# Kernel optimization log

Hardware: AMD Instinct MI355X
Metric: run time of the kernel (lower is better)

Reference implementation:

```python
import jax, jax.numpy as jnp
import numpy as np

GRID_SHAPE = (128, 128, 128, 8)
N_POINTS = 2_000_000


def setup_inputs() -> dict:
    key = jax.random.key(0)
    k1, k2 = jax.random.split(key)
    coords = jax.random.uniform(k1, (N_POINTS, 3), dtype=jnp.float32)
    grid = jax.random.normal(k2, GRID_SHAPE, dtype=jnp.float32)
    bbox_min = jnp.zeros((3,), dtype=jnp.float32)
    bbox_max = jnp.ones((3,), dtype=jnp.float32)
    return {"coords": coords, "grid": grid, "bbox_min": bbox_min, "bbox_max": bbox_max}


def reference(coords, grid, bbox_min, bbox_max):
    # coords: [N, 3]; grid: [X, Y, Z, C]
    eps = 1e-06
    coords = coords[:, :3]
    scale = jnp.maximum(bbox_max - bbox_min, eps)
    normalized = jnp.clip((coords - bbox_min) / scale, 0.0, 1.0)
    grid_size = jnp.asarray(grid.shape[:3], dtype=jnp.int64)  # [3]
    pos = normalized * (grid_size.astype(coords.dtype) - 1.0)  # [N, 3]
    idx0 = jnp.floor(pos).astype(jnp.int64)                    # [N, 3]
    idx1 = jnp.minimum(idx0 + 1, grid_size - 1)                # [N, 3]
    weight = jnp.clip(pos - idx0.astype(coords.dtype), 0.0, 1.0)  # [N, 3]

    x0, y0, z0 = idx0[:, 0], idx0[:, 1], idx0[:, 2]
    x1, y1, z1 = idx1[:, 0], idx1[:, 1], idx1[:, 2]
    wx, wy, wz = weight[:, 0:1], weight[:, 1:2], weight[:, 2:3]  # each [N, 1]

    c000 = grid[x0, y0, z0]
    c100 = grid[x1, y0, z0]
    c010 = grid[x0, y1, z0]
    c110 = grid[x1, y1, z0]
    c001 = grid[x0, y0, z1]
    c101 = grid[x1, y0, z1]
    c011 = grid[x0, y1, z1]
    c111 = grid[x1, y1, z1]

    c00 = c000 * (1.0 - wx) + c100 * wx
    c01 = c001 * (1.0 - wx) + c101 * wx
    c10 = c010 * (1.0 - wx) + c110 * wx
    c11 = c011 * (1.0 - wx) + c111 * wx
    c0 = c00 * (1.0 - wy) + c10 * wy
    c1 = c01 * (1.0 - wy) + c11 * wy
    return c0 * (1.0 - wz) + c1 * wz  # [N, C]
```

## Files before the change

### kernel.cpp

```cpp
#include <hip/hip_runtime.h>


#define GS    128
#define NBX   32
#define NB2   4096
#define CAP1  65536
#define CAP2  704
#define K_PTS 1024
#define HCELLS (5 * 5 * 33)

__device__ __forceinline__ void cell_of(
    float cx, float cy, float cz,
    float b0x, float b0y, float b0z,
    float sx, float sy, float sz,
    int& x0, int& y0, int& z0)
{
    float nx = fminf(fmaxf((cx - b0x) / sx, 0.0f), 1.0f);
    float ny = fminf(fmaxf((cy - b0y) / sy, 0.0f), 1.0f);
    float nz = fminf(fmaxf((cz - b0z) / sz, 0.0f), 1.0f);
    x0 = (int)(nx * (float)(GS - 1));
    y0 = (int)(ny * (float)(GS - 1));
    z0 = (int)(nz * (float)(GS - 1));
}

__global__ __launch_bounds__(256) void k_init(
    unsigned* __restrict__ cursor32, unsigned* __restrict__ cursor4096)
{
    int i = blockIdx.x * 256 + threadIdx.x;
    if (i < NBX) cursor32[i] = (unsigned)i * CAP1;
    if (i < NB2) cursor4096[i] = (unsigned)i * CAP2;
}

__global__ __launch_bounds__(256) void k_scatter1(
    const float* __restrict__ coords,
    const float* __restrict__ bbox_min,
    const float* __restrict__ bbox_max,
    unsigned* __restrict__ cursor32,
    float4* __restrict__ recs1, int n)
{
    __shared__ float4 srec[K_PTS];
    __shared__ unsigned char sbkt[K_PTS];
    __shared__ unsigned cnt[NBX], lbase[NBX], gbase[NBX];

    int t = threadIdx.x;
    if (t < NBX) cnt[t] = 0;
    __syncthreads();

    float b0x = bbox_min[0];
    float sx  = fmaxf(bbox_max[0] - b0x, 1e-6f);
    long long base = (long long)blockIdx.x * K_PTS;
    int m = (int)min((long long)K_PTS, (long long)n - base);

    float cx[4], cy[4], cz[4];
    int bb[4]; unsigned rr[4];
    int j0 = 4 * t;
    if (j0 + 3 < m) {
        const float4* c4 = (const float4*)coords + (size_t)blockIdx.x * 768 + 3 * t;
        float4 f0 = c4[0], f1 = c4[1], f2 = c4[2];
        cx[0] = f0.x; cy[0] = f0.y; cz[0] = f0.z;
        cx[1] = f0.w; cy[1] = f1.x; cz[1] = f1.y;
        cx[2] = f1.z; cy[2] = f1.w; cz[2] = f2.x;
        cx[3] = f2.y; cy[3] = f2.z; cz[3] = f2.w;
    } else {
#pragma unroll
        for (int p = 0; p < 4; ++p) {
            int j = j0 + p;
            if (j < m) {
                long long i = base + j;
                cx[p] = coords[3 * i]; cy[p] = coords[3 * i + 1]; cz[p] = coords[3 * i + 2];
            }
        }
    }
#pragma unroll
    for (int p = 0; p < 4; ++p) {
        int j = j0 + p;
        if (j < m) {
            float nx = fminf(fmaxf((cx[p] - b0x) / sx, 0.0f), 1.0f);
            bb[p] = ((int)(nx * (float)(GS - 1))) >> 2;
            rr[p] = atomicAdd(&cnt[bb[p]], 1u);
        }
    }
    __syncthreads();

    if (t == 0) {
        unsigned acc = 0;
        for (int j = 0; j < NBX; ++j) { lbase[j] = acc; acc += cnt[j]; }
    }
    if (t < NBX && cnt[t]) gbase[t] = atomicAdd(&cursor32[t], cnt[t]);
    __syncthreads();

#pragma unroll
    for (int p = 0; p < 4; ++p) {
        int j = j0 + p;
        if (j < m) {
            unsigned slot = lbase[bb[p]] + rr[p];
            float4 r; r.x = cx[p]; r.y = cy[p]; r.z = cz[p];
            r.w = __uint_as_float((unsigned)(base + j));
            srec[slot] = r;
            sbkt[slot] = (unsigned char)bb[p];
        }
    }
    __syncthreads();

#pragma unroll
    for (int k = 0; k < 4; ++k) {
        int j = k * 256 + t;
        if (j < m) {
            int b = sbkt[j];
            unsigned d = gbase[b] + (unsigned)j - lbase[b];
            if (d < (unsigned)(b + 1) * CAP1) recs1[d] = srec[j];
        }
    }
}

__global__ __launch_bounds__(256) void k_scatter2(
    const float4* __restrict__ recs1,
    const float* __restrict__ bbox_min,
    const float* __restrict__ bbox_max,
    const unsigned* __restrict__ cursor32_final,
    unsigned* __restrict__ cursor4096,
    float4* __restrict__ recs2)
{
    __shared__ float4 srec[K_PTS];
    __shared__ unsigned char sbkt[K_PTS];
    __shared__ unsigned cnt[128], lbase[128], gbase[128];

    int s = blockIdx.x >> 6;
    int c = blockIdx.x & 63;
    unsigned fill = cursor32_final[s] - (unsigned)s * CAP1;
    if (fill > CAP1) fill = CAP1;
    unsigned off = (unsigned)c * 1024;
    if (off >= fill) return;
    int m = (int)min(1024u, fill - off);

    int t = threadIdx.x;
    if (t < 128) cnt[t] = 0;
    __syncthreads();

    float b0x = bbox_min[0], b0y = bbox_min[1], b0z = bbox_min[2];
    float sx = fmaxf(bbox_max[0] - b0x, 1e-6f);
    float sy = fmaxf(bbox_max[1] - b0y, 1e-6f);
    float sz = fmaxf(bbox_max[2] - b0z, 1e-6f);
    long long base = (long long)s * CAP1 + off;

    float4 rc[4]; int bb[4]; unsigned rr[4];
#pragma unroll
    for (int k = 0; k < 4; ++k) {
        int j = k * 256 + t;
        if (j < m) {
            rc[k] = recs1[base + j];
            int x0, y0, z0;
            cell_of(rc[k].x, rc[k].y, rc[k].z, b0x, b0y, b0z, sx, sy, sz, x0, y0, z0);
            bb[k] = ((y0 >> 2) << 2) | (z0 >> 5);
            rr[k] = atomicAdd(&cnt[bb[k]], 1u);
        }
    }
    __syncthreads();

    if (t == 0) {
        unsigned acc = 0;
        for (int j = 0; j < 128; ++j) { lbase[j] = acc; acc += cnt[j]; }
    }
    if (t < 128 && cnt[t]) gbase[t] = atomicAdd(&cursor4096[s * 128 + t], cnt[t]);
    __syncthreads();

#pragma unroll
    for (int k = 0; k < 4; ++k) {
        int j = k * 256 + t;
        if (j < m) {
            unsigned slot = lbase[bb[k]] + rr[k];
            srec[slot] = rc[k];
            sbkt[slot] = (unsigned char)bb[k];
        }
    }
    __syncthreads();

#pragma unroll
    for (int k = 0; k < 4; ++k) {
        int j = k * 256 + t;
        if (j < m) {
            int lb = sbkt[j];
            unsigned g = (unsigned)s * 128 + lb;
            unsigned d = gbase[lb] + (unsigned)j - lbase[lb];
            if (d < (g + 1) * CAP2) recs2[d] = srec[j];
        }
    }
}

__global__ __launch_bounds__(512) void k_interp_staged(
    const float4* __restrict__ recs2,
    const unsigned* __restrict__ cursor4096_final,
    const float* __restrict__ grid,
    const float* __restrict__ bbox_min,
    const float* __restrict__ bbox_max,
    float4* __restrict__ out4)
{
    __shared__ float4 tile[HCELLS * 2];
    __shared__ float4 srec[CAP2];

    int ob = blockIdx.x;
    int b  = (ob & 7) * 512 + (ob >> 3);

    unsigned s0 = (unsigned)b * CAP2;
    unsigned e  = cursor4096_final[b];
    unsigned cap_end = s0 + CAP2;
    if (e > cap_end) e = cap_end;
    if (e <= s0) return;
    int cnt = (int)(e - s0);

    int xs = b >> 7, ys = (b >> 2) & 31, zq = b & 3;
    int t = threadIdx.x;

    for (int k = t; k < cnt; k += 512) srec[k] = recs2[s0 + k];

    const float4* g4 = (const float4*)grid;
    for (int k = t; k < HCELLS * 2; k += 512) {
        int c  = k >> 1, half = k & 1;
        int lx = c / 165;
        int r2 = c - lx * 165;
        int ly = r2 / 33;
        int lz = r2 - ly * 33;
        int gx = min(xs * 4 + lx, GS - 1);
        int gy = min(ys * 4 + ly, GS - 1);
        int gz = min(zq * 32 + lz, GS - 1);
        tile[k] = g4[(((gx * GS) + gy) * GS + gz) * 2 + half];
    }
    __syncthreads();

    const float eps = 1e-6f;
    float b0x = bbox_min[0], b0y = bbox_min[1], b0z = bbox_min[2];
    float sx = fmaxf(bbox_max[0] - b0x, eps);
    float sy = fmaxf(bbox_max[1] - b0y, eps);
    float sz = fmaxf(bbox_max[2] - b0z, eps);

    int pair = t >> 1, half = t & 1;

    for (int cb = 0; cb < cnt; cb += 256) {
        int j = cb + pair;
        if (j >= cnt) continue;
        float4 rec = srec[j];
        unsigned orig = __float_as_uint(rec.w);

        float nx = fminf(fmaxf((rec.x - b0x) / sx, 0.0f), 1.0f);
        float ny = fminf(fmaxf((rec.y - b0y) / sy, 0.0f), 1.0f);
        float nz = fminf(fmaxf((rec.z - b0z) / sz, 0.0f), 1.0f);
        float px = nx * (float)(GS - 1);
        float py = ny * (float)(GS - 1);
        float pz = nz * (float)(GS - 1);
        int x0 = (int)px, y0 = (int)py, z0 = (int)pz;
        int x1 = min(x0 + 1, GS - 1);
        int y1 = min(y0 + 1, GS - 1);
        int z1 = min(z0 + 1, GS - 1);
        float wx = fminf(fmaxf(px - (float)x0, 0.0f), 1.0f);
        float wy = fminf(fmaxf(py - (float)y0, 0.0f), 1.0f);
        float wz = fminf(fmaxf(pz - (float)z0, 0.0f), 1.0f);

        int lx0 = x0 - xs * 4, lx1 = x1 - xs * 4;
        int ly0 = y0 - ys * 4, ly1 = y1 - ys * 4;
        int lz0 = z0 - zq * 32, lz1 = z1 - zq * 32;

        int c000 = ((lx0 * 5 + ly0) * 33 + lz0) * 2 + half;
        int c100 = ((lx1 * 5 + ly0) * 33 + lz0) * 2 + half;
        int c010 = ((lx0 * 5 + ly1) * 33 + lz0) * 2 + half;
        int c110 = ((lx1 * 5 + ly1) * 33 + lz0) * 2 + half;
        int c001 = ((lx0 * 5 + ly0) * 33 + lz1) * 2 + half;
        int c101 = ((lx1 * 5 + ly0) * 33 + lz1) * 2 + half;
        int c011 = ((lx0 * 5 + ly1) * 33 + lz1) * 2 + half;
        int c111 = ((lx1 * 5 + ly1) * 33 + lz1) * 2 + half;

        float ux = 1.0f - wx, uy = 1.0f - wy, uz = 1.0f - wz;
        float w000 = ux*uy*uz, w100 = wx*uy*uz, w010 = ux*wy*uz, w110 = wx*wy*uz;
        float w001 = ux*uy*wz, w101 = wx*uy*wz, w011 = ux*wy*wz, w111 = wx*wy*wz;

        float4 A = tile[c000], B = tile[c100], C = tile[c010], D = tile[c110];
        float4 E = tile[c001], F = tile[c101], H = tile[c011], Kk = tile[c111];

        float4 o;
        o.x = A.x*w000 + B.x*w100 + C.x*w010 + D.x*w110 + E.x*w001 + F.x*w101 + H.x*w011 + Kk.x*w111;
        o.y = A.y*w000 + B.y*w100 + C.y*w010 + D.y*w110 + E.y*w001 + F.y*w101 + H.y*w011 + Kk.y*w111;
        o.z = A.z*w000 + B.z*w100 + C.z*w010 + D.z*w110 + E.z*w001 + F.z*w101 + H.z*w011 + Kk.z*w111;
        o.w = A.w*w000 + B.w*w100 + C.w*w010 + D.w*w110 + E.w*w001 + F.w*w101 + H.w*w011 + Kk.w*w111;

        out4[(long long)orig * 2 + half] = o;
    }
}

__global__ __launch_bounds__(256) void trilerp_direct(
    const float* __restrict__ coords,
    const float* __restrict__ grid,
    const float* __restrict__ bbox_min,
    const float* __restrict__ bbox_max,
    float* __restrict__ out, int n)
{
    int i = blockIdx.x * blockDim.x + threadIdx.x;
    if (i >= n) return;
    const float eps = 1e-6f;
    float b0x = bbox_min[0], b0y = bbox_min[1], b0z = bbox_min[2];
    float sx = fmaxf(bbox_max[0] - b0x, eps);
    float sy = fmaxf(bbox_max[1] - b0y, eps);
    float sz = fmaxf(bbox_max[2] - b0z, eps);
    float nx = fminf(fmaxf((coords[3*i] - b0x) / sx, 0.0f), 1.0f);
    float ny = fminf(fmaxf((coords[3*i+1] - b0y) / sy, 0.0f), 1.0f);
    float nz = fminf(fmaxf((coords[3*i+2] - b0z) / sz, 0.0f), 1.0f);
    float px = nx * (float)(GS - 1), py = ny * (float)(GS - 1), pz = nz * (float)(GS - 1);
    int x0 = (int)px, y0 = (int)py, z0 = (int)pz;
    int x1 = min(x0 + 1, GS - 1), y1 = min(y0 + 1, GS - 1), z1 = min(z0 + 1, GS - 1);
    float wx = fminf(fmaxf(px - (float)x0, 0.0f), 1.0f);
    float wy = fminf(fmaxf(py - (float)y0, 0.0f), 1.0f);
    float wz = fminf(fmaxf(pz - (float)z0, 0.0f), 1.0f);
    float ux = 1.0f - wx, uy = 1.0f - wy, uz = 1.0f - wz;
    float w000 = ux*uy*uz, w100 = wx*uy*uz, w010 = ux*wy*uz, w110 = wx*wy*uz;
    float w001 = ux*uy*wz, w101 = wx*uy*wz, w011 = ux*wy*wz, w111 = wx*wy*wz;
    const float4* g4 = (const float4*)grid;
    int bx0 = x0 * GS, bx1 = x1 * GS;
    int p000 = ((bx0 + y0) * GS + z0) * 2, p100 = ((bx1 + y0) * GS + z0) * 2;
    int p010 = ((bx0 + y1) * GS + z0) * 2, p110 = ((bx1 + y1) * GS + z0) * 2;
    int p001 = ((bx0 + y0) * GS + z1) * 2, p101 = ((bx1 + y0) * GS + z1) * 2;
    int p011 = ((bx0 + y1) * GS + z1) * 2, p111 = ((bx1 + y1) * GS + z1) * 2;
    float4 a0 = g4[p000], a1 = g4[p000+1], b0 = g4[p100], b1 = g4[p100+1];
    float4 c0 = g4[p010], c1 = g4[p010+1], d0 = g4[p110], d1 = g4[p110+1];
    float4 e0 = g4[p001], e1 = g4[p001+1], f0 = g4[p101], f1 = g4[p101+1];
    float4 h0 = g4[p011], h1 = g4[p011+1], k0 = g4[p111], k1 = g4[p111+1];
    float4 o0, o1;
    o0.x = a0.x*w000 + b0.x*w100 + c0.x*w010 + d0.x*w110 + e0.x*w001 + f0.x*w101 + h0.x*w011 + k0.x*w111;
    o0.y = a0.y*w000 + b0.y*w100 + c0.y*w010 + d0.y*w110 + e0.y*w001 + f0.y*w101 + h0.y*w011 + k0.y*w111;
    o0.z = a0.z*w000 + b0.z*w100 + c0.z*w010 + d0.z*w110 + e0.z*w001 + f0.z*w101 + h0.z*w011 + k0.z*w111;
    o0.w = a0.w*w000 + b0.w*w100 + c0.w*w010 + d0.w*w110 + e0.w*w001 + f0.w*w101 + h0.w*w011 + k0.w*w111;
    o1.x = a1.x*w000 + b1.x*w100 + c1.x*w010 + d1.x*w110 + e1.x*w001 + f1.x*w101 + h1.x*w011 + k1.x*w111;
    o1.y = a1.y*w000 + b1.y*w100 + c1.y*w010 + d1.y*w110 + e1.y*w001 + f1.y*w101 + h1.y*w011 + k1.y*w111;
    o1.z = a1.z*w000 + b1.z*w100 + c1.z*w010 + d1.z*w110 + e1.z*w001 + f1.z*w101 + h1.z*w011 + k1.z*w111;
    o1.w = a1.w*w000 + b1.w*w100 + c1.w*w010 + d1.w*w110 + e1.w*w001 + f1.w*w101 + h1.w*w011 + k1.w*w111;
    float4* outp = (float4*)out;
    outp[(long long)i * 2 + 0] = o0;
    outp[(long long)i * 2 + 1] = o1;
}

extern "C" void kernel_launch(void* const* d_in, const int* in_sizes, int n_in,
                              void* d_out, int out_size, void* d_ws, size_t ws_size,
                              hipStream_t stream) {
    const float* coords   = (const float*)d_in[0];
    const float* grid     = (const float*)d_in[1];
    const float* bbox_min = (const float*)d_in[2];
    const float* bbox_max = (const float*)d_in[3];
    float* out = (float*)d_out;

    int n = in_sizes[0] / 3;

    size_t cur32_off = 0;
    size_t cur2_off  = 256;
    size_t recs1_off = 32768;
    size_t recs2_off = recs1_off + (size_t)NBX * CAP1 * 16;
    size_t needed    = recs2_off + (size_t)NB2 * CAP2 * 16;

    int nb_sort = (n + K_PTS - 1) / K_PTS;
    int nb_dir  = (n + 255) / 256;

    if (ws_size >= needed) {
        unsigned* cur32 = (unsigned*)((char*)d_ws + cur32_off);
        unsigned* cur2  = (unsigned*)((char*)d_ws + cur2_off);
        float4*   recs1 = (float4*)((char*)d_ws + recs1_off);
        float4*   recs2 = (float4*)((char*)d_ws + recs2_off);

        k_init    <<<16, 256, 0, stream>>>(cur32, cur2);
        k_scatter1<<<nb_sort, 256, 0, stream>>>(coords, bbox_min, bbox_max, cur32, recs1, n);
        k_scatter2<<<NBX * 64, 256, 0, stream>>>(recs1, bbox_min, bbox_max, cur32, cur2, recs2);
        k_interp_staged<<<NB2, 512, 0, stream>>>(recs2, cur2, grid, bbox_min, bbox_max,
                                                 (float4*)out);
    } else {
        trilerp_direct<<<nb_dir, 256, 0, stream>>>(coords, grid, bbox_min, bbox_max, out, n);
    }
}
```

Before: 94.41 us.

## Write interpolation results in sorted order, then unpermute via recorded positions

The interpolation kernel now writes its outputs contiguously in bucket-sorted order to a temporary buffer instead of scattering 32-byte rows to each point's original index. The scatter kernels record each point's destination slot (pos1, pos2), and a new k_unperm kernel follows the two-level indirection to gather results back into original order with coalesced writes. The aim is to turn scattered output stores into coalesced ones. The cost is an extra kernel launch, extra index traffic, a full extra read and write of the output, and a larger workspace requirement, with the previous path kept as a fallback.

```diff
diff --git a/kernel.cpp b/kernel.cpp
--- a/kernel.cpp
+++ b/kernel.cpp
@@ -8,6 +8,7 @@
 #define CAP2  704
 #define K_PTS 1024
 #define HCELLS (5 * 5 * 33)
+#define UP    8
 
 __device__ __forceinline__ void cell_of(
     float cx, float cy, float cz,
@@ -36,7 +37,9 @@
     const float* __restrict__ bbox_min,
     const float* __restrict__ bbox_max,
     unsigned* __restrict__ cursor32,
-    float4* __restrict__ recs1, int n)
+    float4* __restrict__ recs1,
+    unsigned* __restrict__ pos1,
+    int n)
 {
     __shared__ float4 srec[K_PTS];
     __shared__ unsigned char sbkt[K_PTS];
@@ -98,6 +101,7 @@
             r.w = __uint_as_float((unsigned)(base + j));
             srec[slot] = r;
             sbkt[slot] = (unsigned char)bb[p];
+            if (pos1) pos1[base + j] = gbase[bb[p]] + rr[p];
         }
     }
     __syncthreads();
@@ -119,7 +123,8 @@
     const float* __restrict__ bbox_max,
     const unsigned* __restrict__ cursor32_final,
     unsigned* __restrict__ cursor4096,
-    float4* __restrict__ recs2)
+    float4* __restrict__ recs2,
+    unsigned* __restrict__ pos2)
 {
     __shared__ float4 srec[K_PTS];
     __shared__ unsigned char sbkt[K_PTS];
@@ -171,6 +176,7 @@
             unsigned slot = lbase[bb[k]] + rr[k];
             srec[slot] = rc[k];
             sbkt[slot] = (unsigned char)bb[k];
+            if (pos2) pos2[base + j] = gbase[bb[k]] + rr[k];
         }
     }
     __syncthreads();
@@ -193,7 +199,8 @@
     const float* __restrict__ grid,
     const float* __restrict__ bbox_min,
     const float* __restrict__ bbox_max,
-    float4* __restrict__ out4)
+    float4* __restrict__ dst,
+    int direct_out)
 {
     __shared__ float4 tile[HCELLS * 2];
     __shared__ float4 srec[CAP2];
@@ -281,7 +288,43 @@
         o.z = A.z*w000 + B.z*w100 + C.z*w010 + D.z*w110 + E.z*w001 + F.z*w101 + H.z*w011 + Kk.z*w111;
         o.w = A.w*w000 + B.w*w100 + C.w*w010 + D.w*w110 + E.w*w001 + F.w*w101 + H.w*w011 + Kk.w*w111;
 
-        out4[(long long)orig * 2 + half] = o;
+        long long di = direct_out ? ((long long)orig * 2 + half)
+                                  : ((long long)(s0 + j) * 2 + half);
+        dst[di] = o;
+    }
+}
+
+__global__ __launch_bounds__(512) void k_unperm(
+    const unsigned* __restrict__ pos1,
+    const unsigned* __restrict__ pos2,
+    const float4* __restrict__ tmp4,
+    float4* __restrict__ out4, int n)
+{
+    long long base = (long long)blockIdx.x * (512 * UP);
+    int t = threadIdx.x;
+
+    unsigned d1[UP], d2[UP];
+#pragma unroll
+    for (int p = 0; p < UP; ++p) {
+        long long i = base + (long long)p * 512 + t;
+        d1[p] = (i < n) ? pos1[i] : 0u;
+    }
+#pragma unroll
+    for (int p = 0; p < UP; ++p) d2[p] = pos2[d1[p]];
+
+    float4 v0[UP], v1[UP];
+#pragma unroll
+    for (int p = 0; p < UP; ++p) {
+        v0[p] = tmp4[(long long)d2[p] * 2];
+        v1[p] = tmp4[(long long)d2[p] * 2 + 1];
+    }
+#pragma unroll
+    for (int p = 0; p < UP; ++p) {
+        long long i = base + (long long)p * 512 + t;
+        if (i < n) {
+            out4[i * 2]     = v0[p];
+            out4[i * 2 + 1] = v1[p];
+        }
     }
 }
 
@@ -348,24 +391,45 @@
 
     size_t cur32_off = 0;
     size_t cur2_off  = 256;
-    size_t recs1_off = 32768;
-    size_t recs2_off = recs1_off + (size_t)NBX * CAP1 * 16;
-    size_t needed    = recs2_off + (size_t)NB2 * CAP2 * 16;
+    size_t pos1_off  = 32768;
+    size_t pos2_off  = pos1_off + (size_t)n * 4;
+    size_t recs2_off = pos2_off + (size_t)NBX * CAP1 * 4;
+    size_t union_off = recs2_off + (size_t)NB2 * CAP2 * 16;
+    size_t union_sz  = (size_t)NB2 * CAP2 * 32;
+    size_t needed_full = union_off + union_sz;
+
+    size_t m_recs1_off = 32768;
+    size_t m_recs2_off = m_recs1_off + (size_t)NBX * CAP1 * 16;
+    size_t needed_mid  = m_recs2_off + (size_t)NB2 * CAP2 * 16;
 
     int nb_sort = (n + K_PTS - 1) / K_PTS;
     int nb_dir  = (n + 255) / 256;
 
-    if (ws_size >= needed) {
+    if (ws_size >= needed_full) {
         unsigned* cur32 = (unsigned*)((char*)d_ws + cur32_off);
         unsigned* cur2  = (unsigned*)((char*)d_ws + cur2_off);
-        float4*   recs1 = (float4*)((char*)d_ws + recs1_off);
+        unsigned* pos1  = (unsigned*)((char*)d_ws + pos1_off);
+        unsigned* pos2  = (unsigned*)((char*)d_ws + pos2_off);
         float4*   recs2 = (float4*)((char*)d_ws + recs2_off);
+        float4*   recs1 = (float4*)((char*)d_ws + union_off);
+        float4*   tmp4  = (float4*)((char*)d_ws + union_off);
 
         k_init    <<<16, 256, 0, stream>>>(cur32, cur2);
-        k_scatter1<<<nb_sort, 256, 0, stream>>>(coords, bbox_min, bbox_max, cur32, recs1, n);
-        k_scatter2<<<NBX * 64, 256, 0, stream>>>(recs1, bbox_min, bbox_max, cur32, cur2, recs2);
-        k_interp_staged<<<NB2, 512, 0, stream>>>(recs2, cur2, grid, bbox_min, bbox_max,
-                                                 (float4*)out);
+        k_scatter1<<<nb_sort, 256, 0, stream>>>(coords, bbox_min, bbox_max, cur32, recs1, pos1, n);
+        k_scatter2<<<NBX * 64, 256, 0, stream>>>(recs1, bbox_min, bbox_max, cur32, cur2, recs2, pos2);
+        k_interp_staged<<<NB2, 512, 0, stream>>>(recs2, cur2, grid, bbox_min, bbox_max, tmp4, 0);
+        int nb_up = (int)(((long long)n + 512 * UP - 1) / (512 * UP));
+        k_unperm  <<<nb_up, 512, 0, stream>>>(pos1, pos2, tmp4, (float4*)out, n);
+    } else if (ws_size >= needed_mid) {
+        unsigned* cur32 = (unsigned*)((char*)d_ws + cur32_off);
+        unsigned* cur2  = (unsigned*)((char*)d_ws + cur2_off);
+        float4*   recs1 = (float4*)((char*)d_ws + m_recs1_off);
+        float4*   recs2 = (float4*)((char*)d_ws + m_recs2_off);
+
+        k_init    <<<16, 256, 0, stream>>>(cur32, cur2);
+        k_scatter1<<<nb_sort, 256, 0, stream>>>(coords, bbox_min, bbox_max, cur32, recs1, (unsigned*)0, n);
+        k_scatter2<<<NBX * 64, 256, 0, stream>>>(recs1, bbox_min, bbox_max, cur32, cur2, recs2, (unsigned*)0);
+        k_interp_staged<<<NB2, 512, 0, stream>>>(recs2, cur2, grid, bbox_min, bbox_max, (float4*)out, 1);
     } else {
         trilerp_direct<<<nb_dir, 256, 0, stream>>>(coords, grid, bbox_min, bbox_max, out, n);
     }
```

Measured after the change: 146.1 us. 54.7% more time.

## Partition interpolated outputs by index region before scattering to output

Applied to the files above, without the earlier changes.

The interpolation kernel no longer writes results straight to their scattered original positions. It buckets each result into one of 32 contiguous index regions, using shared-memory atomics and one global cursor per region. A new finalize kernel then reads each region and writes it to the output, so the final writes land in a localized span that should improve write locality and cache behaviour. The cost is an extra full round trip of the 64 MB payload through workspace and one more launch, and the new path only runs when the larger workspace is available.

```diff
diff --git a/kernel.cpp b/kernel.cpp
--- a/kernel.cpp
+++ b/kernel.cpp
@@ -8,6 +8,8 @@
 #define CAP2  704
 #define K_PTS 1024
 #define HCELLS (5 * 5 * 33)
+#define NR    32
+#define RCAP  65536
 
 __device__ __forceinline__ void cell_of(
     float cx, float cy, float cz,
@@ -24,11 +26,13 @@
 }
 
 __global__ __launch_bounds__(256) void k_init(
-    unsigned* __restrict__ cursor32, unsigned* __restrict__ cursor4096)
+    unsigned* __restrict__ cursor32, unsigned* __restrict__ cursor4096,
+    unsigned* __restrict__ cursorR)
 {
     int i = blockIdx.x * 256 + threadIdx.x;
     if (i < NBX) cursor32[i] = (unsigned)i * CAP1;
     if (i < NB2) cursor4096[i] = (unsigned)i * CAP2;
+    if (i < NR)  cursorR[i] = (unsigned)i * RCAP;
 }
 
 __global__ __launch_bounds__(256) void k_scatter1(
@@ -187,16 +191,20 @@
     }
 }
 
-__global__ __launch_bounds__(512) void k_interp_staged(
+__global__ __launch_bounds__(512) void k_interp_part(
     const float4* __restrict__ recs2,
     const unsigned* __restrict__ cursor4096_final,
     const float* __restrict__ grid,
     const float* __restrict__ bbox_min,
     const float* __restrict__ bbox_max,
-    float4* __restrict__ out4)
+    unsigned* __restrict__ cursorR,
+    float4* __restrict__ payR,
+    unsigned* __restrict__ origR)
 {
     __shared__ float4 tile[HCELLS * 2];
-    __shared__ float4 srec[CAP2];
+    __shared__ float4 pay[CAP2 * 2];
+    __shared__ unsigned org[CAP2];
+    __shared__ unsigned rcnt[NR], gbase[NR];
 
     int ob = blockIdx.x;
     int b  = (ob & 7) * 512 + (ob >> 3);
@@ -211,7 +219,7 @@
     int xs = b >> 7, ys = (b >> 2) & 31, zq = b & 3;
     int t = threadIdx.x;
 
-    for (int k = t; k < cnt; k += 512) srec[k] = recs2[s0 + k];
+    if (t < NR) rcnt[t] = 0;
 
     const float4* g4 = (const float4*)grid;
     for (int k = t; k < HCELLS * 2; k += 512) {
@@ -233,12 +241,169 @@
     float sy = fmaxf(bbox_max[1] - b0y, eps);
     float sz = fmaxf(bbox_max[2] - b0z, eps);
 
+    for (int j = t; j < cnt; j += 512) {
+        float4 rec = recs2[s0 + j];
+        unsigned orig = __float_as_uint(rec.w);
+
+        float nx = fminf(fmaxf((rec.x - b0x) / sx, 0.0f), 1.0f);
+        float ny = fminf(fmaxf((rec.y - b0y) / sy, 0.0f), 1.0f);
+        float nz = fminf(fmaxf((rec.z - b0z) / sz, 0.0f), 1.0f);
+        float px = nx * (float)(GS - 1);
+        float py = ny * (float)(GS - 1);
+        float pz = nz * (float)(GS - 1);
+        int x0 = (int)px, y0 = (int)py, z0 = (int)pz;
+        int x1 = min(x0 + 1, GS - 1);
+        int y1 = min(y0 + 1, GS - 1);
+        int z1 = min(z0 + 1, GS - 1);
+        float wx = fminf(fmaxf(px - (float)x0, 0.0f), 1.0f);
+        float wy = fminf(fmaxf(py - (float)y0, 0.0f), 1.0f);
+        float wz = fminf(fmaxf(pz - (float)z0, 0.0f), 1.0f);
+
+        int lx0 = x0 - xs * 4, lx1 = x1 - xs * 4;
+        int ly0 = y0 - ys * 4, ly1 = y1 - ys * 4;
+        int lz0 = z0 - zq * 32, lz1 = z1 - zq * 32;
+
+        int c000 = ((lx0 * 5 + ly0) * 33 + lz0) * 2;
+        int c100 = ((lx1 * 5 + ly0) * 33 + lz0) * 2;
+        int c010 = ((lx0 * 5 + ly1) * 33 + lz0) * 2;
+        int c110 = ((lx1 * 5 + ly1) * 33 + lz0) * 2;
+        int c001 = ((lx0 * 5 + ly0) * 33 + lz1) * 2;
+        int c101 = ((lx1 * 5 + ly0) * 33 + lz1) * 2;
+        int c011 = ((lx0 * 5 + ly1) * 33 + lz1) * 2;
+        int c111 = ((lx1 * 5 + ly1) * 33 + lz1) * 2;
+
+        float ux = 1.0f - wx, uy = 1.0f - wy, uz = 1.0f - wz;
+        float w000 = ux*uy*uz, w100 = wx*uy*uz, w010 = ux*wy*uz, w110 = wx*wy*uz;
+        float w001 = ux*uy*wz, w101 = wx*uy*wz, w011 = ux*wy*wz, w111 = wx*wy*wz;
+
+        float4 A0 = tile[c000], A1 = tile[c000 + 1];
+        float4 B0 = tile[c100], B1 = tile[c100 + 1];
+        float4 C0 = tile[c010], C1 = tile[c010 + 1];
+        float4 D0 = tile[c110], D1 = tile[c110 + 1];
+        float4 E0 = tile[c001], E1 = tile[c001 + 1];
+        float4 F0 = tile[c101], F1 = tile[c101 + 1];
+        float4 H0 = tile[c011], H1 = tile[c011 + 1];
+        float4 K0 = tile[c111], K1 = tile[c111 + 1];
+
+        float4 o0, o1;
+        o0.x = A0.x*w000 + B0.x*w100 + C0.x*w010 + D0.x*w110 + E0.x*w001 + F0.x*w101 + H0.x*w011 + K0.x*w111;
+        o0.y = A0.y*w000 + B0.y*w100 + C0.y*w010 + D0.y*w110 + E0.y*w001 + F0.y*w101 + H0.y*w011 + K0.y*w111;
+        o0.z = A0.z*w000 + B0.z*w100 + C0.z*w010 + D0.z*w110 + E0.z*w001 + F0.z*w101 + H0.z*w011 + K0.z*w111;
+        o0.w = A0.w*w000 + B0.w*w100 + C0.w*w010 + D0.w*w110 + E0.w*w001 + F0.w*w101 + H0.w*w011 + K0.w*w111;
+        o1.x = A1.x*w000 + B1.x*w100 + C1.x*w010 + D1.x*w110 + E1.x*w001 + F1.x*w101 + H1.x*w011 + K1.x*w111;
+        o1.y = A1.y*w000 + B1.y*w100 + C1.y*w010 + D1.y*w110 + E1.y*w001 + F1.y*w101 + H1.y*w011 + K1.y*w111;
+        o1.z = A1.z*w000 + B1.z*w100 + C1.z*w010 + D1.z*w110 + E1.z*w001 + F1.z*w101 + H1.z*w011 + K1.z*w111;
+        o1.w = A1.w*w000 + B1.w*w100 + C1.w*w010 + D1.w*w110 + E1.w*w001 + F1.w*w101 + H1.w*w011 + K1.w*w111;
+
+        pay[j * 2]     = o0;
+        pay[j * 2 + 1] = o1;
+        unsigned r = orig >> 16;
+        unsigned rank = atomicAdd(&rcnt[r], 1u);
+        org[j] = orig | (rank << 21);
+    }
+    __syncthreads();
+
+    if (t < NR && rcnt[t]) gbase[t] = atomicAdd(&cursorR[t], rcnt[t]);
+    __syncthreads();
+
+    for (int j = t; j < cnt; j += 512) {
+        unsigned meta = org[j];
+        unsigned orig = meta & 0x1FFFFFu;
+        unsigned rank = meta >> 21;
+        unsigned r = orig >> 16;
+        unsigned dst = gbase[r] + rank;
+        payR[(size_t)dst * 2]     = pay[j * 2];
+        payR[(size_t)dst * 2 + 1] = pay[j * 2 + 1];
+        origR[dst] = orig;
+    }
+}
+
+__global__ __launch_bounds__(1024) void k_finalize(
+    const float4* __restrict__ payR,
+    const unsigned* __restrict__ origR,
+    float4* __restrict__ out4, int n)
+{
+    int b = blockIdx.x;
+    int region = (b & 7) * 4 + ((b >> 3) & 3);
+    int sub = b >> 5;
+    long long rstart = (long long)region * RCAP;
+    long long cr = (long long)n - rstart;
+    int cnt_r = (int)min((long long)RCAP, cr < 0 ? 0LL : cr);
+    int base = sub * (RCAP / 8);
+    int t = threadIdx.x;
+
+    unsigned og[8]; float4 v0[8], v1[8]; int ok[8];
+#pragma unroll
+    for (int p = 0; p < 8; ++p) {
+        int k = base + p * 1024 + t;
+        ok[p] = (k < cnt_r);
+        long long idx = rstart + k;
+        if (ok[p]) og[p] = origR[idx];
+    }
+#pragma unroll
+    for (int p = 0; p < 8; ++p) {
+        int k = base + p * 1024 + t;
+        long long idx = rstart + k;
+        if (ok[p]) { v0[p] = payR[idx * 2]; v1[p] = payR[idx * 2 + 1]; }
+    }
+#pragma unroll
+    for (int p = 0; p < 8; ++p) {
+        if (ok[p]) {
+            long long d = (long long)og[p] * 2;
+            out4[d]     = v0[p];
+            out4[d + 1] = v1[p];
+        }
+    }
+}
+
+__global__ __launch_bounds__(512) void k_interp_direct(
+    const float4* __restrict__ recs2,
+    const unsigned* __restrict__ cursor4096_final,
+    const float* __restrict__ grid,
+    const float* __restrict__ bbox_min,
+    const float* __restrict__ bbox_max,
+    float4* __restrict__ out4)
+{
+    __shared__ float4 tile[HCELLS * 2];
+
+    int ob = blockIdx.x;
+    int b  = (ob & 7) * 512 + (ob >> 3);
+
+    unsigned s0 = (unsigned)b * CAP2;
+    unsigned e  = cursor4096_final[b];
+    unsigned cap_end = s0 + CAP2;
+    if (e > cap_end) e = cap_end;
+    if (e <= s0) return;
+    int cnt = (int)(e - s0);
+
+    int xs = b >> 7, ys = (b >> 2) & 31, zq = b & 3;
+    int t = threadIdx.x;
+
+    const float4* g4 = (const float4*)grid;
+    for (int k = t; k < HCELLS * 2; k += 512) {
+        int c  = k >> 1, half = k & 1;
+        int lx = c / 165;
+        int r2 = c - lx * 165;
+        int ly = r2 / 33;
+        int lz = r2 - ly * 33;
+        int gx = min(xs * 4 + lx, GS - 1);
+        int gy = min(ys * 4 + ly, GS - 1);
+        int gz = min(zq * 32 + lz, GS - 1);
+        tile[k] = g4[(((gx * GS) + gy) * GS + gz) * 2 + half];
+    }
+    __syncthreads();
+
+    const float eps = 1e-6f;
+    float b0x = bbox_min[0], b0y = bbox_min[1], b0z = bbox_min[2];
+    float sx = fmaxf(bbox_max[0] - b0x, eps);
+    float sy = fmaxf(bbox_max[1] - b0y, eps);
+    float sz = fmaxf(bbox_max[2] - b0z, eps);
+
     int pair = t >> 1, half = t & 1;
-
     for (int cb = 0; cb < cnt; cb += 256) {
         int j = cb + pair;
         if (j >= cnt) continue;
-        float4 rec = srec[j];
+        float4 rec = recs2[s0 + j];
         unsigned orig = __float_as_uint(rec.w);
 
         float nx = fminf(fmaxf((rec.x - b0x) / sx, 0.0f), 1.0f);
@@ -348,23 +513,47 @@
 
     size_t cur32_off = 0;
     size_t cur2_off  = 256;
-    size_t recs1_off = 32768;
-    size_t recs2_off = recs1_off + (size_t)NBX * CAP1 * 16;
-    size_t needed    = recs2_off + (size_t)NB2 * CAP2 * 16;
+    size_t curR_off  = 20480;
+    size_t payR_off  = 65536;
+    size_t payR_sz   = (size_t)NR * RCAP * 32;
+    size_t recs2_off = payR_off + payR_sz;
+    size_t recs2_sz  = (size_t)NB2 * CAP2 * 16;
+    size_t origR_off = recs2_off + recs2_sz;
+    size_t needed_full = origR_off + (size_t)NR * RCAP * 4;
+
+    size_t m_recs1_off = 65536;
+    size_t m_recs2_off = m_recs1_off + (size_t)NBX * CAP1 * 16;
+    size_t needed_mid  = m_recs2_off + recs2_sz;
 
     int nb_sort = (n + K_PTS - 1) / K_PTS;
     int nb_dir  = (n + 255) / 256;
 
-    if (ws_size >= needed) {
+    if (ws_size >= needed_full) {
         unsigned* cur32 = (unsigned*)((char*)d_ws + cur32_off);
         unsigned* cur2  = (unsigned*)((char*)d_ws + cur2_off);
-        float4*   recs1 = (float4*)((char*)d_ws + recs1_off);
+        unsigned* curR  = (unsigned*)((char*)d_ws + curR_off);
+        float4*   recs1 = (float4*)((char*)d_ws + payR_off);
+        float4*   payR  = (float4*)((char*)d_ws + payR_off);
         float4*   recs2 = (float4*)((char*)d_ws + recs2_off);
-
-        k_init    <<<16, 256, 0, stream>>>(cur32, cur2);
+        unsigned* origR = (unsigned*)((char*)d_ws + origR_off);
+
+        k_init    <<<16, 256, 0, stream>>>(cur32, cur2, curR);
         k_scatter1<<<nb_sort, 256, 0, stream>>>(coords, bbox_min, bbox_max, cur32, recs1, n);
         k_scatter2<<<NBX * 64, 256, 0, stream>>>(recs1, bbox_min, bbox_max, cur32, cur2, recs2);
-        k_interp_staged<<<NB2, 512, 0, stream>>>(recs2, cur2, grid, bbox_min, bbox_max,
+        k_interp_part<<<NB2, 512, 0, stream>>>(recs2, cur2, grid, bbox_min, bbox_max,
+                                               curR, payR, origR);
+        k_finalize<<<NR * 8, 1024, 0, stream>>>(payR, origR, (float4*)out, n);
+    } else if (ws_size >= needed_mid) {
+        unsigned* cur32 = (unsigned*)((char*)d_ws + cur32_off);
+        unsigned* cur2  = (unsigned*)((char*)d_ws + cur2_off);
+        unsigned* curR  = (unsigned*)((char*)d_ws + curR_off);
+        float4*   recs1 = (float4*)((char*)d_ws + m_recs1_off);
+        float4*   recs2 = (float4*)((char*)d_ws + m_recs2_off);
+
+        k_init    <<<16, 256, 0, stream>>>(cur32, cur2, curR);
+        k_scatter1<<<nb_sort, 256, 0, stream>>>(coords, bbox_min, bbox_max, cur32, recs1, n);
+        k_scatter2<<<NBX * 64, 256, 0, stream>>>(recs1, bbox_min, bbox_max, cur32, cur2, recs2);
+        k_interp_direct<<<NB2, 512, 0, stream>>>(recs2, cur2, grid, bbox_min, bbox_max,
                                                  (float4*)out);
     } else {
         trilerp_direct<<<nb_dir, 256, 0, stream>>>(coords, grid, bbox_min, bbox_max, out, n);
```

Result: slower. 198.4 us (+110.1%).
